# Kernel optimization log

Measured on AMD Instinct MI355X. Metric: run time of the kernel, lower is better.

The kernel has to match this reference:

```python
import jax, jax.numpy as jnp
import numpy as np

T, H, I, E, K = 4096, 2048, 2816, 8, 2


def setup_inputs() -> dict:
    key = jax.random.key(0)
    k1, k2, k3, k4, k5 = jax.random.split(key, 5)
    x = jax.random.normal(k1, (T, H), dtype=jnp.float32)
    w13 = jax.random.normal(k2, (E, 2 * I, H), dtype=jnp.float32) * 0.02
    w2 = jax.random.normal(k3, (E, H, I), dtype=jnp.float32) * 0.02
    topk_weights = jax.random.uniform(k4, (T, K), dtype=jnp.float32)
    topk_ids = jax.random.randint(k5, (T, K), 0, E, dtype=jnp.int64)
    return {"x": x, "w13": w13, "w2": w2, "topk_weights": topk_weights, "topk_ids": topk_ids}


def reference(x, w13, w2, topk_weights, topk_ids):
    # SwiGLU MoE: per expert e, y_e = silu(x @ w1g_e^T) * (x @ w1u_e^T) @ w2_e^T
    # then combine with routing weights for the top-k selected experts.
    w_gate = w13[:, :I, :]   # [E, I, H]
    w_up = w13[:, I:, :]     # [E, I, H]
    gate = jnp.einsum('th,eih->eti', x, w_gate)  # [E, T, I]
    up = jnp.einsum('th,eih->eti', x, w_up)      # [E, T, I]
    act = jax.nn.silu(gate) * up                 # [E, T, I]
    y = jnp.einsum('eti,ehi->eth', act, w2)      # [E, T, H]
    # combine[t, e] = sum_k topk_weights[t, k] * (topk_ids[t, k] == e)
    onehot = (topk_ids[:, :, None] == jnp.arange(E)[None, None, :]).astype(x.dtype)  # [T, K, E]
    combine = jnp.einsum('tk,tke->te', topk_weights, onehot)  # [T, E]
    out = jnp.einsum('eth,te->th', y, combine)   # [T, H]
    return out
```

## Files before the change

### kernel.cpp

```cpp
#include <hip/hip_runtime.h>
#include <hip/hip_bf16.h>

#define TT 4096
#define HH 2048
#define CI 2816
#define EE 8
#define KK 2
#define TKN (TT * KK)
#define TM 128
#define BK 64
#define MAX_MT (TKN / TM + EE)
#define ROWS_PAD (MAX_MT * TM)

typedef short short8 __attribute__((ext_vector_type(8)));
typedef float floatx4 __attribute__((ext_vector_type(4)));

__device__ __forceinline__ unsigned short f2bf(float f) {
  unsigned u = __float_as_uint(f);
  return (unsigned short)((u + 0x8000u) >> 16);
}

__device__ __forceinline__ void cvt_store8(unsigned short* dst, float4 a, float4 b) {
  short8 v;
  v[0] = (short)f2bf(a.x); v[1] = (short)f2bf(a.y);
  v[2] = (short)f2bf(a.z); v[3] = (short)f2bf(a.w);
  v[4] = (short)f2bf(b.x); v[5] = (short)f2bf(b.y);
  v[6] = (short)f2bf(b.z); v[7] = (short)f2bf(b.w);
  *(short8*)dst = v;
}

__device__ __forceinline__ void gload_lds16(const unsigned short* g, unsigned short* l) {
  __builtin_amdgcn_global_load_lds(
      (const __attribute__((address_space(1))) unsigned int*)g,
      (__attribute__((address_space(3))) unsigned int*)l, 16, 0, 0);
}

__global__ void cvt_kernel(const float* __restrict__ src, unsigned short* __restrict__ dst,
                           int n8) {
  for (int i = blockIdx.x * blockDim.x + threadIdx.x; i < n8; i += gridDim.x * blockDim.x) {
    float4 a = ((const float4*)src)[2 * i];
    float4 b = ((const float4*)src)[2 * i + 1];
    cvt_store8(dst + (size_t)i * 8, a, b);
  }
}

__global__ void bucket_kernel(const int* __restrict__ ids, const float* __restrict__ tw,
                              int* __restrict__ hdr, int* __restrict__ tok,
                              float* __restrict__ wt) {
  __shared__ int cnt[EE];
  __shared__ int cur[EE];
  int tid = threadIdx.x;
  if (tid < EE) cnt[tid] = 0;
  __syncthreads();
  for (int p = tid; p < TKN; p += 256) atomicAdd(&cnt[ids[p]], 1);
  for (int r = tid; r < ROWS_PAD; r += 256) { tok[r] = 0; wt[r] = 0.f; }
  __syncthreads();
  if (tid == 0) {
    int rb = 0, tb = 0;
    for (int e = 0; e < EE; e++) {
      cur[e] = rb;
      int nt = (cnt[e] + TM - 1) / TM;
      for (int j = 0; j < nt; j++) hdr[1 + tb + j] = e;
      rb += nt * TM;
      tb += nt;
    }
    for (int m = tb; m < MAX_MT; m++) hdr[1 + m] = 0;
    hdr[0] = tb;
  }
  __syncthreads();
  for (int p = tid; p < TKN; p += 256) {
    int e = ids[p];
    int slot = atomicAdd(&cur[e], 1);
    tok[slot] = p / KK;
    wt[slot] = tw[p];
  }
}

__global__ __launch_bounds__(256, 2)
void gemm1_kernel(const unsigned short* __restrict__ xb, const unsigned short* __restrict__ w13b,
                  const int* __restrict__ hdr, const int* __restrict__ tok,
                  unsigned short* __restrict__ act) {
  const int mt = blockIdx.x;
  if (mt >= hdr[0]) return;
  const int e = hdr[1 + mt];
  const int bn = blockIdx.y;
  const int row_base = mt * TM;
  const int tid = threadIdx.x;
  const int lane = tid & 63;
  const int wave = tid >> 6;

  __shared__ __align__(16) unsigned short As[TM][BK];
  __shared__ __align__(16) unsigned short Bs[TM][BK];

  const int kcol = (lane & 7) * 8;
  const unsigned short* gA[4];
  const unsigned short* gB[4];
  unsigned short* lA[4];
  unsigned short* lB[4];
#pragma unroll
  for (int j = 0; j < 4; j++) {
    int r = wave * 32 + j * 8 + (lane >> 3);
    gA[j] = xb + (size_t)tok[row_base + r] * HH + kcol;
    int wrow = (r < 64) ? (bn * 64 + r) : (CI + bn * 64 + (r - 64));
    gB[j] = w13b + ((size_t)e * (2 * CI) + wrow) * HH + kcol;
    lA[j] = &As[wave * 32 + j * 8][0];
    lB[j] = &Bs[wave * 32 + j * 8][0];
  }

  floatx4 acc[2][8];
#pragma unroll
  for (int mi = 0; mi < 2; mi++)
#pragma unroll
    for (int ni = 0; ni < 8; ni++) acc[mi][ni] = (floatx4){0.f, 0.f, 0.f, 0.f};

  const int lrow = lane & 15;
  const int quad = lane >> 4;
  const int m0 = wave * 32;

  for (int k0 = 0; k0 < HH; k0 += BK) {
    __syncthreads();
#pragma unroll
    for (int j = 0; j < 4; j++) {
      gload_lds16(gA[j] + k0, lA[j]);
      gload_lds16(gB[j] + k0, lB[j]);
    }
    __syncthreads();
#pragma unroll
    for (int kh = 0; kh < 2; kh++) {
      short8 af0 = *(const short8*)&As[m0 + lrow][kh * 32 + quad * 8];
      short8 af1 = *(const short8*)&As[m0 + 16 + lrow][kh * 32 + quad * 8];
#pragma unroll
      for (int ni = 0; ni < 8; ni++) {
        short8 bf = *(const short8*)&Bs[ni * 16 + lrow][kh * 32 + quad * 8];
        acc[0][ni] = __builtin_amdgcn_mfma_f32_16x16x32_bf16(af0, bf, acc[0][ni], 0, 0, 0);
        acc[1][ni] = __builtin_amdgcn_mfma_f32_16x16x32_bf16(af1, bf, acc[1][ni], 0, 0, 0);
      }
    }
  }

  const int col0 = bn * 64;
#pragma unroll
  for (int mi = 0; mi < 2; mi++) {
#pragma unroll
    for (int ni = 0; ni < 4; ni++) {
#pragma unroll
      for (int r = 0; r < 4; r++) {
        float g = acc[mi][ni][r];
        float uu = acc[mi][ni + 4][r];
        float s = g / (1.f + __expf(-g));
        int row = row_base + m0 + mi * 16 + quad * 4 + r;
        int col = col0 + ni * 16 + lrow;
        act[(size_t)row * CI + col] = f2bf(s * uu);
      }
    }
  }
}

__global__ __launch_bounds__(256, 2)
void gemm2_kernel(const unsigned short* __restrict__ act, const unsigned short* __restrict__ w2b,
                  const int* __restrict__ hdr, const int* __restrict__ tok,
                  const float* __restrict__ wt, float* __restrict__ out) {
  const int mt = blockIdx.x;
  if (mt >= hdr[0]) return;
  const int e = hdr[1 + mt];
  const int h0 = blockIdx.y * TM;
  const int row_base = mt * TM;
  const int tid = threadIdx.x;
  const int lane = tid & 63;
  const int wave = tid >> 6;

  __shared__ __align__(16) unsigned short As[TM][BK];
  __shared__ __align__(16) unsigned short Bs[TM][BK];
  __shared__ int tok_s[TM];
  __shared__ float wt_s[TM];

  if (tid < TM) {
    tok_s[tid] = tok[row_base + tid];
    wt_s[tid] = wt[row_base + tid];
  }

  const int kcol = (lane & 7) * 8;
  const unsigned short* gA[4];
  const unsigned short* gB[4];
  unsigned short* lA[4];
  unsigned short* lB[4];
#pragma unroll
  for (int j = 0; j < 4; j++) {
    int r = wave * 32 + j * 8 + (lane >> 3);
    gA[j] = act + (size_t)(row_base + r) * CI + kcol;
    gB[j] = w2b + ((size_t)e * HH + h0 + r) * CI + kcol;
    lA[j] = &As[wave * 32 + j * 8][0];
    lB[j] = &Bs[wave * 32 + j * 8][0];
  }

  floatx4 acc[2][8];
#pragma unroll
  for (int mi = 0; mi < 2; mi++)
#pragma unroll
    for (int ni = 0; ni < 8; ni++) acc[mi][ni] = (floatx4){0.f, 0.f, 0.f, 0.f};

  const int lrow = lane & 15;
  const int quad = lane >> 4;
  const int m0 = wave * 32;

  for (int k0 = 0; k0 < CI; k0 += BK) {
    __syncthreads();
#pragma unroll
    for (int j = 0; j < 4; j++) {
      gload_lds16(gA[j] + k0, lA[j]);
      gload_lds16(gB[j] + k0, lB[j]);
    }
    __syncthreads();
#pragma unroll
    for (int kh = 0; kh < 2; kh++) {
      short8 af0 = *(const short8*)&As[m0 + lrow][kh * 32 + quad * 8];
      short8 af1 = *(const short8*)&As[m0 + 16 + lrow][kh * 32 + quad * 8];
#pragma unroll
      for (int ni = 0; ni < 8; ni++) {
        short8 bf = *(const short8*)&Bs[ni * 16 + lrow][kh * 32 + quad * 8];
        acc[0][ni] = __builtin_amdgcn_mfma_f32_16x16x32_bf16(af0, bf, acc[0][ni], 0, 0, 0);
        acc[1][ni] = __builtin_amdgcn_mfma_f32_16x16x32_bf16(af1, bf, acc[1][ni], 0, 0, 0);
      }
    }
  }

#pragma unroll
  for (int mi = 0; mi < 2; mi++) {
#pragma unroll
    for (int ni = 0; ni < 8; ni++) {
#pragma unroll
      for (int r = 0; r < 4; r++) {
        int lr = m0 + mi * 16 + quad * 4 + r;
        float w = wt_s[lr];
        if (w != 0.f) {
          atomicAdd(out + (size_t)tok_s[lr] * HH + h0 + ni * 16 + lrow, acc[mi][ni][r] * w);
        }
      }
    }
  }
}

extern "C" void kernel_launch(void* const* d_in, const int* in_sizes, int n_in,
                              void* d_out, int out_size, void* d_ws, size_t ws_size,
                              hipStream_t stream) {
  const float* x   = (const float*)d_in[0];
  const float* w13 = (const float*)d_in[1];
  const float* w2  = (const float*)d_in[2];
  const float* tw  = (const float*)d_in[3];
  const int*   ids = (const int*)d_in[4];
  float* out = (float*)d_out;

  char* ws = (char*)d_ws;
  int* hdr = (int*)ws;
  int* tok = (int*)(ws + 512);
  float* wt = (float*)(ws + 512 + ROWS_PAD * 4);
  unsigned short* act  = (unsigned short*)(ws + 74240);
  unsigned short* xb   = (unsigned short*)(ws + 74240 + 51904512ull);
  unsigned short* w13b = (unsigned short*)(ws + 74240 + 51904512ull + 16777216ull);
  unsigned short* w2b  = (unsigned short*)(ws + 74240 + 51904512ull + 16777216ull + 184549376ull);

  hipMemsetAsync(d_out, 0, (size_t)out_size * sizeof(float), stream);
  bucket_kernel<<<1, 256, 0, stream>>>(ids, tw, hdr, tok, wt);
  cvt_kernel<<<2048, 256, 0, stream>>>(x, xb, TT * HH / 8);
  cvt_kernel<<<4096, 256, 0, stream>>>(w13, w13b, EE * 2 * CI * HH / 8);
  cvt_kernel<<<4096, 256, 0, stream>>>(w2, w2b, EE * HH * CI / 8);
  gemm1_kernel<<<dim3(MAX_MT, CI / 64), 256, 0, stream>>>(xb, w13b, hdr, tok, act);
  gemm2_kernel<<<dim3(MAX_MT, HH / TM), 256, 0, stream>>>(act, w2b, hdr, tok, wt, out);
}
```

Measured before the change: 1.194 ms.

## Rewrite grouped GEMMs with 256x128 tiles, 4-stage LDS pipeline, and separate combine

Both expert GEMMs move to 512-thread blocks with 256-row tiles, XOR-swizzled LDS, a 4-deep global-to-LDS prefetch pipeline with explicit waitcnt/barriers and setprio, plus an XCD-aware block remap. The atomic scatter-add epilogue is replaced by writing per-slot outputs to a buffer, followed by a combine kernel that gathers the two routed rows per token using an inverse slot map. This drops the output memset and atomics. In exchange it uses more padding rows and an extra pass over a large fp32 intermediate, and the y buffer aliases w13b, which is safe only because gemm1 finishes before gemm2 writes.

```diff
diff --git a/kernel.cpp b/kernel.cpp
--- a/kernel.cpp
+++ b/kernel.cpp
@@ -1,5 +1,4 @@
 #include <hip/hip_runtime.h>
-#include <hip/hip_bf16.h>
 
 #define TT 4096
 #define HH 2048
@@ -7,13 +6,14 @@
 #define EE 8
 #define KK 2
 #define TKN (TT * KK)
-#define TM 128
-#define BK 64
+#define TM 256
 #define MAX_MT (TKN / TM + EE)
 #define ROWS_PAD (MAX_MT * TM)
 
 typedef short short8 __attribute__((ext_vector_type(8)));
 typedef float floatx4 __attribute__((ext_vector_type(4)));
+
+#define MFMA_B16(a, b, c) __builtin_amdgcn_mfma_f32_16x16x32_bf16(a, b, c, 0, 0, 0)
 
 __device__ __forceinline__ unsigned short f2bf(float f) {
   unsigned u = __float_as_uint(f);
@@ -35,6 +35,11 @@
       (__attribute__((address_space(3))) unsigned int*)l, 16, 0, 0);
 }
 
+__device__ __forceinline__ short8 lds_frag(const unsigned short* base, int row, int quad) {
+  const int off = row * 64 + ((quad * 16) ^ ((row & 3) << 4));
+  return *(const short8*)((const char*)base + off);
+}
+
 __global__ void cvt_kernel(const float* __restrict__ src, unsigned short* __restrict__ dst,
                            int n8) {
   for (int i = blockIdx.x * blockDim.x + threadIdx.x; i < n8; i += gridDim.x * blockDim.x) {
@@ -44,16 +49,16 @@
   }
 }
 
-__global__ void bucket_kernel(const int* __restrict__ ids, const float* __restrict__ tw,
+__global__ void bucket_kernel(const int* __restrict__ ids,
                               int* __restrict__ hdr, int* __restrict__ tok,
-                              float* __restrict__ wt) {
+                              int* __restrict__ inv) {
   __shared__ int cnt[EE];
   __shared__ int cur[EE];
   int tid = threadIdx.x;
   if (tid < EE) cnt[tid] = 0;
   __syncthreads();
   for (int p = tid; p < TKN; p += 256) atomicAdd(&cnt[ids[p]], 1);
-  for (int r = tid; r < ROWS_PAD; r += 256) { tok[r] = 0; wt[r] = 0.f; }
+  for (int r = tid; r < ROWS_PAD; r += 256) tok[r] = 0;
   __syncthreads();
   if (tid == 0) {
     int rb = 0, tb = 0;
@@ -72,171 +77,229 @@
     int e = ids[p];
     int slot = atomicAdd(&cur[e], 1);
     tok[slot] = p / KK;
-    wt[slot] = tw[p];
-  }
-}
-
-__global__ __launch_bounds__(256, 2)
+    inv[p] = slot;
+  }
+}
+
+#define KLOOP_BODY(T_, STAGE_, WAITN_)                                                   \
+  {                                                                                      \
+    const int t_ = (T_);                                                                 \
+    const int slot_ = t_ & 3;                                                            \
+    const unsigned short* As_ = &smem[slot_][0][0];                                      \
+    const unsigned short* Bs_ = &smem[slot_][1][0];                                      \
+    short8 a_[8];                                                                        \
+    _Pragma("unroll")                                                                    \
+    for (int m_ = 0; m_ < 8; ++m_)                                                       \
+      a_[m_] = lds_frag(As_, wr * 128 + m_ * 16 + lrow, quad);                           \
+    short8 b0_ = lds_frag(Bs_, wc * 64 + lrow, quad);                                    \
+    short8 b1_ = lds_frag(Bs_, wc * 64 + 16 + lrow, quad);                               \
+    if (STAGE_) { STAGE_A(t_ + 3); }                                                     \
+    __builtin_amdgcn_s_barrier();                                                        \
+    asm volatile("s_waitcnt lgkmcnt(0)" ::: "memory");                                   \
+    __builtin_amdgcn_sched_barrier(0);                                                   \
+    __builtin_amdgcn_s_setprio(1);                                                       \
+    _Pragma("unroll")                                                                    \
+    for (int m_ = 0; m_ < 8; ++m_) {                                                     \
+      acc[m_][0] = MFMA_B16(a_[m_], b0_, acc[m_][0]);                                    \
+      acc[m_][1] = MFMA_B16(a_[m_], b1_, acc[m_][1]);                                    \
+    }                                                                                    \
+    __builtin_amdgcn_s_setprio(0);                                                       \
+    __builtin_amdgcn_sched_barrier(0);                                                   \
+    __builtin_amdgcn_s_barrier();                                                        \
+    short8 b2_ = lds_frag(Bs_, wc * 64 + 32 + lrow, quad);                               \
+    short8 b3_ = lds_frag(Bs_, wc * 64 + 48 + lrow, quad);                               \
+    if (STAGE_) { STAGE_B(t_ + 3); }                                                     \
+    __builtin_amdgcn_s_barrier();                                                        \
+    asm volatile("s_waitcnt lgkmcnt(0)" ::: "memory");                                   \
+    __builtin_amdgcn_sched_barrier(0);                                                   \
+    __builtin_amdgcn_s_setprio(1);                                                       \
+    _Pragma("unroll")                                                                    \
+    for (int m_ = 0; m_ < 8; ++m_) {                                                     \
+      acc[m_][2] = MFMA_B16(a_[m_], b2_, acc[m_][2]);                                    \
+      acc[m_][3] = MFMA_B16(a_[m_], b3_, acc[m_][3]);                                    \
+    }                                                                                    \
+    __builtin_amdgcn_s_setprio(0);                                                       \
+    __builtin_amdgcn_sched_barrier(0);                                                   \
+    if ((WAITN_) == 8)      asm volatile("s_waitcnt vmcnt(8)" ::: "memory");             \
+    else if ((WAITN_) == 4) asm volatile("s_waitcnt vmcnt(4)" ::: "memory");             \
+    else if ((WAITN_) == 0) asm volatile("s_waitcnt vmcnt(0)" ::: "memory");             \
+    __builtin_amdgcn_s_barrier();                                                        \
+  }
+
+__global__ __launch_bounds__(512, 2)
 void gemm1_kernel(const unsigned short* __restrict__ xb, const unsigned short* __restrict__ w13b,
                   const int* __restrict__ hdr, const int* __restrict__ tok,
                   unsigned short* __restrict__ act) {
-  const int mt = blockIdx.x;
+  const int nwg = MAX_MT * (CI / 128);
+  int orig = blockIdx.y * MAX_MT + blockIdx.x;
+  int id = (orig & 7) * (nwg >> 3) + (orig >> 3);
+  const int mt = id / (CI / 128);
+  const int bn = id % (CI / 128);
   if (mt >= hdr[0]) return;
   const int e = hdr[1 + mt];
-  const int bn = blockIdx.y;
   const int row_base = mt * TM;
+
   const int tid = threadIdx.x;
   const int lane = tid & 63;
   const int wave = tid >> 6;
-
-  __shared__ __align__(16) unsigned short As[TM][BK];
-  __shared__ __align__(16) unsigned short Bs[TM][BK];
-
-  const int kcol = (lane & 7) * 8;
-  const unsigned short* gA[4];
-  const unsigned short* gB[4];
-  unsigned short* lA[4];
-  unsigned short* lB[4];
-#pragma unroll
-  for (int j = 0; j < 4; j++) {
-    int r = wave * 32 + j * 8 + (lane >> 3);
-    gA[j] = xb + (size_t)tok[row_base + r] * HH + kcol;
-    int wrow = (r < 64) ? (bn * 64 + r) : (CI + bn * 64 + (r - 64));
-    gB[j] = w13b + ((size_t)e * (2 * CI) + wrow) * HH + kcol;
-    lA[j] = &As[wave * 32 + j * 8][0];
-    lB[j] = &Bs[wave * 32 + j * 8][0];
-  }
-
-  floatx4 acc[2][8];
-#pragma unroll
-  for (int mi = 0; mi < 2; mi++)
-#pragma unroll
-    for (int ni = 0; ni < 8; ni++) acc[mi][ni] = (floatx4){0.f, 0.f, 0.f, 0.f};
-
+  const int wr = wave >> 2;
+  const int wc = wave & 3;
   const int lrow = lane & 15;
   const int quad = lane >> 4;
-  const int m0 = wave * 32;
-
-  for (int k0 = 0; k0 < HH; k0 += BK) {
-    __syncthreads();
-#pragma unroll
-    for (int j = 0; j < 4; j++) {
-      gload_lds16(gA[j] + k0, lA[j]);
-      gload_lds16(gB[j] + k0, lB[j]);
-    }
-    __syncthreads();
-#pragma unroll
-    for (int kh = 0; kh < 2; kh++) {
-      short8 af0 = *(const short8*)&As[m0 + lrow][kh * 32 + quad * 8];
-      short8 af1 = *(const short8*)&As[m0 + 16 + lrow][kh * 32 + quad * 8];
-#pragma unroll
-      for (int ni = 0; ni < 8; ni++) {
-        short8 bf = *(const short8*)&Bs[ni * 16 + lrow][kh * 32 + quad * 8];
-        acc[0][ni] = __builtin_amdgcn_mfma_f32_16x16x32_bf16(af0, bf, acc[0][ni], 0, 0, 0);
-        acc[1][ni] = __builtin_amdgcn_mfma_f32_16x16x32_bf16(af1, bf, acc[1][ni], 0, 0, 0);
+
+  __shared__ __align__(16) unsigned short smem[4][2][8192];
+
+  const int r0 = tid >> 2;
+  const int cph = (tid & 3) * 16;
+  const int cs = cph ^ ((r0 & 3) << 4);
+
+  const char* sA0 = (const char*)(xb + (size_t)tok[row_base + r0] * HH) + cs;
+  const char* sA1 = (const char*)(xb + (size_t)tok[row_base + r0 + 128] * HH) + cs;
+  const char* sB0;
+  const char* sB1;
+  {
+    int l0 = r0 & 63, g0 = r0 >> 6;
+    int wrow0 = (l0 < 32) ? (bn * 128 + g0 * 32 + l0) : (CI + bn * 128 + g0 * 32 + (l0 - 32));
+    sB0 = (const char*)(w13b + ((size_t)e * (2 * CI) + wrow0) * HH) + cs;
+    int r1 = r0 + 128;
+    int l1 = r1 & 63, g1 = r1 >> 6;
+    int wrow1 = (l1 < 32) ? (bn * 128 + g1 * 32 + l1) : (CI + bn * 128 + g1 * 32 + (l1 - 32));
+    sB1 = (const char*)(w13b + ((size_t)e * (2 * CI) + wrow1) * HH) + cs;
+  }
+
+  auto STAGE_A = [&](int tt) {
+    int s = tt & 3;
+    gload_lds16((const unsigned short*)(sA0 + (size_t)tt * 64), &smem[s][0][wave * 512]);
+    gload_lds16((const unsigned short*)(sA1 + (size_t)tt * 64), &smem[s][0][4096 + wave * 512]);
+  };
+  auto STAGE_B = [&](int tt) {
+    int s = tt & 3;
+    gload_lds16((const unsigned short*)(sB0 + (size_t)tt * 64), &smem[s][1][wave * 512]);
+    gload_lds16((const unsigned short*)(sB1 + (size_t)tt * 64), &smem[s][1][4096 + wave * 512]);
+  };
+
+  floatx4 acc[8][4];
+#pragma unroll
+  for (int m = 0; m < 8; ++m)
+#pragma unroll
+    for (int n = 0; n < 4; ++n) acc[m][n] = (floatx4){0.f, 0.f, 0.f, 0.f};
+
+  STAGE_A(0); STAGE_B(0); STAGE_A(1); STAGE_B(1); STAGE_A(2); STAGE_B(2);
+  asm volatile("s_waitcnt vmcnt(8)" ::: "memory");
+  __builtin_amdgcn_s_barrier();
+
+  const int NT = HH / 32;
+  for (int t = 0; t < NT - 3; ++t) KLOOP_BODY(t, 1, 8);
+  KLOOP_BODY(NT - 3, 0, 4);
+  KLOOP_BODY(NT - 2, 0, 0);
+  KLOOP_BODY(NT - 1, 0, -1);
+
+  const int colb = bn * 128 + wc * 32;
+#pragma unroll
+  for (int m = 0; m < 8; ++m) {
+    const int row = row_base + wr * 128 + m * 16 + quad * 4;
+#pragma unroll
+    for (int n = 0; n < 2; ++n) {
+#pragma unroll
+      for (int r = 0; r < 4; ++r) {
+        float g = acc[m][n][r];
+        float u = acc[m][n + 2][r];
+        float s = g / (1.f + __expf(-g));
+        act[(size_t)(row + r) * CI + colb + n * 16 + lrow] = f2bf(s * u);
       }
     }
   }
-
-  const int col0 = bn * 64;
-#pragma unroll
-  for (int mi = 0; mi < 2; mi++) {
-#pragma unroll
-    for (int ni = 0; ni < 4; ni++) {
-#pragma unroll
-      for (int r = 0; r < 4; r++) {
-        float g = acc[mi][ni][r];
-        float uu = acc[mi][ni + 4][r];
-        float s = g / (1.f + __expf(-g));
-        int row = row_base + m0 + mi * 16 + quad * 4 + r;
-        int col = col0 + ni * 16 + lrow;
-        act[(size_t)row * CI + col] = f2bf(s * uu);
-      }
-    }
-  }
-}
-
-__global__ __launch_bounds__(256, 2)
+}
+
+__global__ __launch_bounds__(512, 2)
 void gemm2_kernel(const unsigned short* __restrict__ act, const unsigned short* __restrict__ w2b,
-                  const int* __restrict__ hdr, const int* __restrict__ tok,
-                  const float* __restrict__ wt, float* __restrict__ out) {
-  const int mt = blockIdx.x;
+                  const int* __restrict__ hdr, float* __restrict__ y) {
+  const int nwg = MAX_MT * (HH / 256);
+  int orig = blockIdx.y * MAX_MT + blockIdx.x;
+  int id = (orig & 7) * (nwg >> 3) + (orig >> 3);
+  const int mt = id / (HH / 256);
+  const int bh = id % (HH / 256);
   if (mt >= hdr[0]) return;
   const int e = hdr[1 + mt];
-  const int h0 = blockIdx.y * TM;
   const int row_base = mt * TM;
+  const int h0 = bh * 256;
+
   const int tid = threadIdx.x;
   const int lane = tid & 63;
   const int wave = tid >> 6;
-
-  __shared__ __align__(16) unsigned short As[TM][BK];
-  __shared__ __align__(16) unsigned short Bs[TM][BK];
-  __shared__ int tok_s[TM];
-  __shared__ float wt_s[TM];
-
-  if (tid < TM) {
-    tok_s[tid] = tok[row_base + tid];
-    wt_s[tid] = wt[row_base + tid];
-  }
-
-  const int kcol = (lane & 7) * 8;
-  const unsigned short* gA[4];
-  const unsigned short* gB[4];
-  unsigned short* lA[4];
-  unsigned short* lB[4];
-#pragma unroll
-  for (int j = 0; j < 4; j++) {
-    int r = wave * 32 + j * 8 + (lane >> 3);
-    gA[j] = act + (size_t)(row_base + r) * CI + kcol;
-    gB[j] = w2b + ((size_t)e * HH + h0 + r) * CI + kcol;
-    lA[j] = &As[wave * 32 + j * 8][0];
-    lB[j] = &Bs[wave * 32 + j * 8][0];
-  }
-
-  floatx4 acc[2][8];
-#pragma unroll
-  for (int mi = 0; mi < 2; mi++)
-#pragma unroll
-    for (int ni = 0; ni < 8; ni++) acc[mi][ni] = (floatx4){0.f, 0.f, 0.f, 0.f};
-
+  const int wr = wave >> 2;
+  const int wc = wave & 3;
   const int lrow = lane & 15;
   const int quad = lane >> 4;
-  const int m0 = wave * 32;
-
-  for (int k0 = 0; k0 < CI; k0 += BK) {
-    __syncthreads();
-#pragma unroll
-    for (int j = 0; j < 4; j++) {
-      gload_lds16(gA[j] + k0, lA[j]);
-      gload_lds16(gB[j] + k0, lB[j]);
-    }
-    __syncthreads();
-#pragma unroll
-    for (int kh = 0; kh < 2; kh++) {
-      short8 af0 = *(const short8*)&As[m0 + lrow][kh * 32 + quad * 8];
-      short8 af1 = *(const short8*)&As[m0 + 16 + lrow][kh * 32 + quad * 8];
-#pragma unroll
-      for (int ni = 0; ni < 8; ni++) {
-        short8 bf = *(const short8*)&Bs[ni * 16 + lrow][kh * 32 + quad * 8];
-        acc[0][ni] = __builtin_amdgcn_mfma_f32_16x16x32_bf16(af0, bf, acc[0][ni], 0, 0, 0);
-        acc[1][ni] = __builtin_amdgcn_mfma_f32_16x16x32_bf16(af1, bf, acc[1][ni], 0, 0, 0);
+
+  __shared__ __align__(16) unsigned short smem[4][2][8192];
+
+  const int r0 = tid >> 2;
+  const int cph = (tid & 3) * 16;
+  const int cs = cph ^ ((r0 & 3) << 4);
+
+  const char* sA0 = (const char*)(act + (size_t)(row_base + r0) * CI) + cs;
+  const char* sA1 = (const char*)(act + (size_t)(row_base + r0 + 128) * CI) + cs;
+  const char* sB0 = (const char*)(w2b + ((size_t)e * HH + h0 + r0) * CI) + cs;
+  const char* sB1 = (const char*)(w2b + ((size_t)e * HH + h0 + r0 + 128) * CI) + cs;
+
+  auto STAGE_A = [&](int tt) {
+    int s = tt & 3;
+    gload_lds16((const unsigned short*)(sA0 + (size_t)tt * 64), &smem[s][0][wave * 512]);
+    gload_lds16((const unsigned short*)(sA1 + (size_t)tt * 64), &smem[s][0][4096 + wave * 512]);
+  };
+  auto STAGE_B = [&](int tt) {
+    int s = tt & 3;
+    gload_lds16((const unsigned short*)(sB0 + (size_t)tt * 64), &smem[s][1][wave * 512]);
+    gload_lds16((const unsigned short*)(sB1 + (size_t)tt * 64), &smem[s][1][4096 + wave * 512]);
+  };
+
+  floatx4 acc[8][4];
+#pragma unroll
+  for (int m = 0; m < 8; ++m)
+#pragma unroll
+    for (int n = 0; n < 4; ++n) acc[m][n] = (floatx4){0.f, 0.f, 0.f, 0.f};
+
+  STAGE_A(0); STAGE_B(0); STAGE_A(1); STAGE_B(1); STAGE_A(2); STAGE_B(2);
+  asm volatile("s_waitcnt vmcnt(8)" ::: "memory");
+  __builtin_amdgcn_s_barrier();
+
+  const int NT = CI / 32;
+  for (int t = 0; t < NT - 3; ++t) KLOOP_BODY(t, 1, 8);
+  KLOOP_BODY(NT - 3, 0, 4);
+  KLOOP_BODY(NT - 2, 0, 0);
+  KLOOP_BODY(NT - 1, 0, -1);
+
+#pragma unroll
+  for (int m = 0; m < 8; ++m) {
+    const int row = row_base + wr * 128 + m * 16 + quad * 4;
+#pragma unroll
+    for (int n = 0; n < 4; ++n) {
+#pragma unroll
+      for (int r = 0; r < 4; ++r) {
+        y[(size_t)(row + r) * HH + h0 + wc * 64 + n * 16 + lrow] = acc[m][n][r];
       }
     }
   }
-
-#pragma unroll
-  for (int mi = 0; mi < 2; mi++) {
-#pragma unroll
-    for (int ni = 0; ni < 8; ni++) {
-#pragma unroll
-      for (int r = 0; r < 4; r++) {
-        int lr = m0 + mi * 16 + quad * 4 + r;
-        float w = wt_s[lr];
-        if (w != 0.f) {
-          atomicAdd(out + (size_t)tok_s[lr] * HH + h0 + ni * 16 + lrow, acc[mi][ni][r] * w);
-        }
-      }
-    }
+}
+
+__global__ __launch_bounds__(256)
+void combine_kernel(const float* __restrict__ y, const float* __restrict__ tw,
+                    const int* __restrict__ inv, float* __restrict__ out) {
+  const int t = blockIdx.x;
+  const int s0 = inv[2 * t], s1 = inv[2 * t + 1];
+  const float w0 = tw[2 * t], w1 = tw[2 * t + 1];
+  const float4* y0 = (const float4*)(y + (size_t)s0 * HH);
+  const float4* y1 = (const float4*)(y + (size_t)s1 * HH);
+  float4* o = (float4*)(out + (size_t)t * HH);
+  for (int c = threadIdx.x; c < HH / 4; c += 256) {
+    float4 a = y0[c], b = y1[c];
+    float4 v;
+    v.x = w0 * a.x + w1 * b.x;
+    v.y = w0 * a.y + w1 * b.y;
+    v.z = w0 * a.z + w1 * b.z;
+    v.w = w0 * a.w + w1 * b.w;
+    o[c] = v;
   }
 }
 
@@ -253,17 +316,18 @@
   char* ws = (char*)d_ws;
   int* hdr = (int*)ws;
   int* tok = (int*)(ws + 512);
-  float* wt = (float*)(ws + 512 + ROWS_PAD * 4);
+  int* inv = (int*)(ws + 41472);
   unsigned short* act  = (unsigned short*)(ws + 74240);
-  unsigned short* xb   = (unsigned short*)(ws + 74240 + 51904512ull);
-  unsigned short* w13b = (unsigned short*)(ws + 74240 + 51904512ull + 16777216ull);
-  unsigned short* w2b  = (unsigned short*)(ws + 74240 + 51904512ull + 16777216ull + 184549376ull);
-
-  hipMemsetAsync(d_out, 0, (size_t)out_size * sizeof(float), stream);
-  bucket_kernel<<<1, 256, 0, stream>>>(ids, tw, hdr, tok, wt);
+  unsigned short* xb   = (unsigned short*)(ws + 57745920ull);
+  unsigned short* w13b = (unsigned short*)(ws + 74523136ull);
+  unsigned short* w2b  = (unsigned short*)(ws + 259072512ull);
+  float* y = (float*)(ws + 74523136ull);
+
+  bucket_kernel<<<1, 256, 0, stream>>>(ids, hdr, tok, inv);
   cvt_kernel<<<2048, 256, 0, stream>>>(x, xb, TT * HH / 8);
   cvt_kernel<<<4096, 256, 0, stream>>>(w13, w13b, EE * 2 * CI * HH / 8);
   cvt_kernel<<<4096, 256, 0, stream>>>(w2, w2b, EE * HH * CI / 8);
-  gemm1_kernel<<<dim3(MAX_MT, CI / 64), 256, 0, stream>>>(xb, w13b, hdr, tok, act);
-  gemm2_kernel<<<dim3(MAX_MT, HH / TM), 256, 0, stream>>>(act, w2b, hdr, tok, wt, out);
-}
+  gemm1_kernel<<<dim3(MAX_MT, CI / 128), 512, 0, stream>>>(xb, w13b, hdr, tok, act);
+  gemm2_kernel<<<dim3(MAX_MT, HH / 256), 512, 0, stream>>>(act, w2b, hdr, y);
+  combine_kernel<<<TT, 256, 0, stream>>>(y, tw, inv, out);
+}
```

Result: faster. 1.131 ms (-5.2%).
